# Performance work log

Hardware: AMD Instinct MI355X
Metric: run time of the kernel (lower is better)

## Reference

```python
import jax, jax.numpy as jnp
import numpy as np

B, N, K, H, D = 2, 8192, 16, 4, 32
C_IN, C_OUT = 64, 128
HD = H * D


def setup_inputs() -> dict:
    key = jax.random.key(0)
    ks = jax.random.split(key, 16)
    s = 0.02
    return {
        "xyzs": jax.random.normal(ks[0], (B, N, 3), jnp.float32),
        "features": jax.random.normal(ks[1], (B, N, C_IN), jnp.float32),
        "k_graph": jax.random.randint(ks[2], (B, N, K), 0, N),
        # projections (stored as [in, out]; torch Linear applies x @ W.T)
        "Wk": jax.random.normal(ks[3], (C_IN, HD), jnp.float32) * s,
        "Wv": jax.random.normal(ks[4], (C_IN, HD), jnp.float32) * s,
        "Wq": jax.random.normal(ks[5], (C_IN, HD), jnp.float32) * s,
        # aggregate MLP: Linear(HD,HD) -> ReLU -> Linear(HD,H)
        "A1": jax.random.normal(ks[6], (HD, HD), jnp.float32) * s,
        "b1": jnp.zeros((HD,), jnp.float32),
        "A2": jax.random.normal(ks[7], (HD, H), jnp.float32) * s,
        "b2": jnp.zeros((H,), jnp.float32),
        # position MLP: Linear(3,3) -> ReLU -> Linear(3,HD)
        "P1": jax.random.normal(ks[8], (3, 3), jnp.float32) * s,
        "bp1": jnp.zeros((3,), jnp.float32),
        "P2": jax.random.normal(ks[9], (3, HD), jnp.float32) * s,
        "bp2": jnp.zeros((HD,), jnp.float32),
        # output projection Linear(HD, C_OUT)
        "Wout": jax.random.normal(ks[10], (HD, C_OUT), jnp.float32) * s,
        "bout": jnp.zeros((C_OUT,), jnp.float32),
    }


def reference(xyzs, features, k_graph, Wk, Wv, Wq, A1, b1, A2, b2,
              P1, bp1, P2, bp2, Wout, bout):
    # KNN gather (irregular access): [B,N,K,*]
    nbr_feat = jax.vmap(lambda f, g: f[g])(features, k_graph)   # [B,N,K,C_IN]
    nbr_xyz = jax.vmap(lambda x, g: x[g])(xyzs, k_graph)        # [B,N,K,3]

    rel_pos = xyzs[:, :, None, :] - nbr_xyz                      # [B,N,K,3]
    pe = jax.nn.relu(rel_pos @ P1 + bp1) @ P2 + bp2              # [B,N,K,HD]

    keys = nbr_feat @ Wk                                         # [B,N,K,HD]
    values = nbr_feat @ Wv                                       # [B,N,K,HD]
    queries = features @ Wq                                      # [B,N,HD]

    # subtraction attention + aggregate MLP -> per-head logits
    attn = queries[:, :, None, :] - keys + pe                    # [B,N,K,HD]
    attn = jax.nn.relu(attn @ A1 + b1) @ A2 + b2                 # [B,N,K,H]
    attn = jax.nn.softmax(attn, axis=-2)                         # softmax over K

    # weighted reduce over neighbors
    fv = (values + pe).reshape(B, N, K, H, D)
    fused = jnp.sum(attn[..., None] * fv, axis=2)                # [B,N,H,D]
    fused = fused.reshape(B, N, HD)
    return fused @ Wout + bout                                   # [B,N,C_OUT]
```

## Files before the change

### kernel.cpp

```cpp
#include <hip/hip_runtime.h>
#include <hip/hip_bf16.h>

#define BATCH 2
#define NPTS  8192
#define BN    (BATCH * NPTS)
#define KNN   16
#define HEADS 4
#define HD    128
#define CIN   64
#define COUT  128
#define WCOLS 384

using short8  = __attribute__((ext_vector_type(8))) short;
using float4v = __attribute__((ext_vector_type(4))) float;
using float2v = __attribute__((ext_vector_type(2))) float;

static __device__ __forceinline__ unsigned short f2bf(float x) {
    unsigned u = __float_as_uint(x);
    u += 0x7fffu + ((u >> 16) & 1u);
    return (unsigned short)(u >> 16);
}
static __device__ __forceinline__ float bf_lo(unsigned u) { return __uint_as_float(u << 16); }
static __device__ __forceinline__ float bf_hi(unsigned u) { return __uint_as_float(u & 0xffff0000u); }
static __device__ __forceinline__ unsigned pack2(float a, float b) {
    return (unsigned)f2bf(a) | ((unsigned)f2bf(b) << 16);
}
static __device__ __forceinline__ float2v bf2pair(unsigned u) {
    float2v r;
    r.x = __uint_as_float(u << 16);
    r.y = __uint_as_float(u & 0xffff0000u);
    return r;
}

static __device__ __forceinline__ float2v pk_add(float2v a, float2v b) {
    float2v d;
    asm("v_pk_add_f32 %0, %1, %2" : "=v"(d) : "v"(a), "v"(b));
    return d;
}
static __device__ __forceinline__ float2v pk_sub(float2v a, float2v b) {
    float2v d;
    asm("v_pk_add_f32 %0, %1, %2 neg_lo:[0,1] neg_hi:[0,1]" : "=v"(d) : "v"(a), "v"(b));
    return d;
}
static __device__ __forceinline__ float2v pk_mul(float2v a, float2v b) {
    float2v d;
    asm("v_pk_mul_f32 %0, %1, %2" : "=v"(d) : "v"(a), "v"(b));
    return d;
}
static __device__ __forceinline__ float2v pk_fma(float2v a, float2v b, float2v c) {
    float2v d;
    asm("v_pk_fma_f32 %0, %1, %2, %3" : "=v"(d) : "v"(a), "v"(b), "v"(c));
    return d;
}
static __device__ __forceinline__ float2v sx2(float2v v, int mask) {
    float2v r;
    r.x = __shfl_xor(v.x, mask, 64);
    r.y = __shfl_xor(v.y, mask, 64);
    return r;
}

template <int CTRL>
static __device__ __forceinline__ float dpp_mov(float x) {
    return __int_as_float(
        __builtin_amdgcn_update_dpp(0, __float_as_int(x), CTRL, 0xf, 0xf, false));
}
static __device__ __forceinline__ float ror_sum16(float x) {
    x += dpp_mov<0x128>(x);
    x += dpp_mov<0x124>(x);
    x += dpp_mov<0x122>(x);
    x += dpp_mov<0x121>(x);
    return x;
}
static __device__ __forceinline__ float ror_max16(float x) {
    x = fmaxf(x, dpp_mov<0x128>(x));
    x = fmaxf(x, dpp_mov<0x124>(x));
    x = fmaxf(x, dpp_mov<0x122>(x));
    x = fmaxf(x, dpp_mov<0x121>(x));
    return x;
}

__global__ void prep_kernel(const float* __restrict__ Wk,
                            const float* __restrict__ Wv,
                            const float* __restrict__ Wq,
                            const float* __restrict__ A1,
                            const float* __restrict__ b1,
                            const float* __restrict__ P2,
                            const float* __restrict__ bp2,
                            const float* __restrict__ Wout,
                            unsigned short* __restrict__ WcatT,
                            unsigned short* __restrict__ WoutT,
                            float* __restrict__ P2A1,
                            float* __restrict__ cvec) {
    int t = blockIdx.x * blockDim.x + threadIdx.x;
    if (t < WCOLS * CIN) {
        int n = t >> 6, kk = t & 63;
        float val;
        if (n < 2 * HD) {
            const float* w = (n < HD ? Wq : Wk) + kk * HD;
            int jj = n & (HD - 1);
            float acc = 0.f;
            #pragma unroll 4
            for (int m = 0; m < HD; m += 4) {
                float4 wr = *(const float4*)(w + m);
                acc += wr.x * A1[(m+0)*HD + jj] + wr.y * A1[(m+1)*HD + jj]
                     + wr.z * A1[(m+2)*HD + jj] + wr.w * A1[(m+3)*HD + jj];
            }
            val = acc;
        } else {
            val = Wv[kk * HD + (n - 2 * HD)];
        }
        WcatT[t] = f2bf(val);
    } else if (t < WCOLS * CIN + COUT * HD) {
        int u = t - WCOLS * CIN;
        int n = u >> 7, kk = u & 127;
        WoutT[u] = f2bf(Wout[kk * COUT + n]);
    } else if (t < WCOLS * CIN + COUT * HD + 3 * HD) {
        int u = t - (WCOLS * CIN + COUT * HD);
        int r = u / HD, j = u % HD;
        const float* w = P2 + r * HD;
        float acc = 0.f;
        #pragma unroll 4
        for (int m = 0; m < HD; m += 4) {
            float4 wr = *(const float4*)(w + m);
            acc += wr.x * A1[(m+0)*HD + j] + wr.y * A1[(m+1)*HD + j]
                 + wr.z * A1[(m+2)*HD + j] + wr.w * A1[(m+3)*HD + j];
        }
        P2A1[u] = acc;
    } else if (t < WCOLS * CIN + COUT * HD + 3 * HD + HD) {
        int j = t - (WCOLS * CIN + COUT * HD + 3 * HD);
        float acc = b1[j];
        #pragma unroll 4
        for (int m = 0; m < HD; m += 4) {
            float4 wr = *(const float4*)(bp2 + m);
            acc += wr.x * A1[(m+0)*HD + j] + wr.y * A1[(m+1)*HD + j]
                 + wr.z * A1[(m+2)*HD + j] + wr.w * A1[(m+3)*HD + j];
        }
        cvec[j] = acc;
    }
}

#define AK 88
__global__ __launch_bounds__(256) void qkv_kernel(const float* __restrict__ F,
                                                  const unsigned short* __restrict__ WcatT,
                                                  const float* __restrict__ cvec,
                                                  unsigned short* __restrict__ QKVb) {
    __shared__ unsigned short Af[64 * AK];
    __shared__ unsigned short Bf[WCOLS * AK];
    int p0 = blockIdx.x * 64;
    int t = threadIdx.x;

    #pragma unroll
    for (int i = 0; i < 4; ++i) {
        int v = t + i * 256;
        int row = v >> 4, c4 = (v & 15) * 4;
        float4 fa = *(const float4*)(F + (p0 + row) * CIN + c4);
        uint2 u = make_uint2(pack2(fa.x, fa.y), pack2(fa.z, fa.w));
        *(uint2*)(&Af[row * AK + c4]) = u;
    }
    #pragma unroll
    for (int i = 0; i < 12; ++i) {
        int v = t + i * 256;
        int n = v >> 3, j16 = v & 7;
        *(uint4*)(&Bf[n * AK + j16 * 8]) = ((const uint4*)WcatT)[v];
    }
    __syncthreads();

    int w = t >> 6, l = t & 63;
    int ml = l & 15, quad = l >> 4;
    int m0 = w * 16;

    short8 a0 = *(const short8*)(&Af[(m0 + ml) * AK + quad * 8]);
    short8 a1 = *(const short8*)(&Af[(m0 + ml) * AK + 32 + quad * 8]);

    #pragma unroll
    for (int nt = 0; nt < 24; ++nt) {
        short8 b0 = *(const short8*)(&Bf[(nt * 16 + ml) * AK + quad * 8]);
        short8 b1 = *(const short8*)(&Bf[(nt * 16 + ml) * AK + 32 + quad * 8]);
        float4v acc = {0.f, 0.f, 0.f, 0.f};
        acc = __builtin_amdgcn_mfma_f32_16x16x32_bf16(a0, b0, acc, 0, 0, 0);
        acc = __builtin_amdgcn_mfma_f32_16x16x32_bf16(a1, b1, acc, 0, 0, 0);
        int n = nt * 16 + ml;
        float cadd = (n < HD) ? cvec[n] : 0.f;
        #pragma unroll
        for (int r = 0; r < 4; ++r) {
            int row = p0 + m0 + quad * 4 + r;
            QKVb[row * WCOLS + n] = f2bf(acc[r] + cadd);
        }
    }
}

__global__ __launch_bounds__(256) void attn_kernel(
        const float* __restrict__ xyzs, const int* __restrict__ kg,
        const unsigned short* __restrict__ QKVb,
        const float* __restrict__ P1, const float* __restrict__ bp1,
        const float* __restrict__ P2, const float* __restrict__ bp2,
        const float* __restrict__ P2A1,
        const float* __restrict__ A2, const float* __restrict__ b2,
        unsigned short* __restrict__ FUSEDb) {
    __shared__ float4 A2pA[64];
    __shared__ float4 A2pB[64];
    __shared__ float4 WApA[64];
    __shared__ float2 WApB[64];
    __shared__ float4 P2s[HD];
    int t = threadIdx.x;
    if (t < 64) {
        int c = t * 2;
        float4 a2l = *(const float4*)(A2 + c * 4);
        float4 a2h = *(const float4*)(A2 + (c + 1) * 4);
        A2pA[t] = make_float4(a2l.x, a2h.x, a2l.y, a2h.y);
        A2pB[t] = make_float4(a2l.z, a2h.z, a2l.w, a2h.w);
        WApA[t] = make_float4(P2A1[c], P2A1[c + 1], P2A1[HD + c], P2A1[HD + c + 1]);
        WApB[t] = make_float2(P2A1[2 * HD + c], P2A1[2 * HD + c + 1]);
    }
    if (t < HD) P2s[t] = make_float4(P2[t], P2[HD + t], P2[2 * HD + t], bp2[t]);
    __syncthreads();

    int lane = t & 63;
    int p = blockIdx.x * 4 + (t >> 6);
    int b = p >> 13;
    int k = lane & 15, cg = lane >> 4;
    int c0 = cg * 32;

    int idx = kg[p * KNN + k];
    int q = b * NPTS + idx;

    float r0 = xyzs[p * 3 + 0] - xyzs[q * 3 + 0];
    float r1 = xyzs[p * 3 + 1] - xyzs[q * 3 + 1];
    float r2 = xyzs[p * 3 + 2] - xyzs[q * 3 + 2];
    float h0 = fmaxf(r0 * P1[0] + r1 * P1[3] + r2 * P1[6] + bp1[0], 0.f);
    float h1 = fmaxf(r0 * P1[1] + r1 * P1[4] + r2 * P1[7] + bp1[1], 0.f);
    float h2 = fmaxf(r0 * P1[2] + r1 * P1[5] + r2 * P1[8] + bp1[2], 0.f);

    const uint4* qp = (const uint4*)(QKVb + (size_t)p * WCOLS + c0);
    const uint4* kp = (const uint4*)(QKVb + (size_t)q * WCOLS + HD + c0);
    const uint4* vp = (const uint4*)(QKVb + (size_t)q * WCOLS + 2 * HD + c0);
    uint4 quA[4] = {qp[0], qp[1], qp[2], qp[3]};
    uint4 kuA[4] = {kp[0], kp[1], kp[2], kp[3]};
    uint4 vuA[4] = {vp[0], vp[1], vp[2], vp[3]};

    float2v h0p = {h0, h0}, h1p = {h1, h1}, h2p = {h2, h2};
    float2v pl0 = {0.f, 0.f}, pl1 = {0.f, 0.f}, pl2 = {0.f, 0.f}, pl3 = {0.f, 0.f};
    int pbase = cg * 16;

    #pragma unroll
    for (int jc = 0; jc < 4; ++jc) {
        const unsigned* uq = (const unsigned*)&quA[jc];
        const unsigned* uk = (const unsigned*)&kuA[jc];
        #pragma unroll
        for (int jp = 0; jp < 4; ++jp) {
            float2v qp2 = bf2pair(uq[jp]);
            float2v kp2 = bf2pair(uk[jp]);
            int pi = pbase + jc * 4 + jp;
            float4 wa = WApA[pi];
            float2 wb = WApB[pi];
            float2v acc = pk_sub(qp2, kp2);
            acc = pk_fma(h0p, (float2v){wa.x, wa.y}, acc);
            acc = pk_fma(h1p, (float2v){wa.z, wa.w}, acc);
            acc = pk_fma(h2p, (float2v){wb.x, wb.y}, acc);
            float2v z2;
            z2.x = fmaxf(acc.x, 0.f);
            z2.y = fmaxf(acc.y, 0.f);
            float4 aA = A2pA[pi], aB = A2pB[pi];
            pl0 = pk_fma(z2, (float2v){aA.x, aA.y}, pl0);
            pl1 = pk_fma(z2, (float2v){aA.z, aA.w}, pl1);
            pl2 = pk_fma(z2, (float2v){aB.x, aB.y}, pl2);
            pl3 = pk_fma(z2, (float2v){aB.z, aB.w}, pl3);
        }
    }
    float l0 = pl0.x + pl0.y;
    float l1 = pl1.x + pl1.y;
    float l2 = pl2.x + pl2.y;
    float l3 = pl3.x + pl3.y;

    l0 += __shfl_xor(l0, 16, 64); l0 += __shfl_xor(l0, 32, 64);
    l1 += __shfl_xor(l1, 16, 64); l1 += __shfl_xor(l1, 32, 64);
    l2 += __shfl_xor(l2, 16, 64); l2 += __shfl_xor(l2, 32, 64);
    l3 += __shfl_xor(l3, 16, 64); l3 += __shfl_xor(l3, 32, 64);

    float lgt = l0;
    lgt = (cg == 1) ? l1 : lgt;
    lgt = (cg == 2) ? l2 : lgt;
    lgt = (cg == 3) ? l3 : lgt;

    float m16 = ror_max16(lgt);
    float e = __expf(lgt - m16);
    float s = ror_sum16(e);
    float a = e / s;

    float hb0 = ror_sum16(a * h0);
    float hb1 = ror_sum16(a * h1);
    float hb2 = ror_sum16(a * h2);

    float2v ap = {a, a};
    float2v y0[4], y1[4], y2[4], y3[4];
    {
        const unsigned* v0 = (const unsigned*)&vuA[0];
        const unsigned* v1 = (const unsigned*)&vuA[1];
        const unsigned* v2 = (const unsigned*)&vuA[2];
        const unsigned* v3 = (const unsigned*)&vuA[3];
        #pragma unroll
        for (int i = 0; i < 4; ++i) {
            y0[i] = pk_mul(ap, bf2pair(v0[i]));
            y1[i] = pk_mul(ap, bf2pair(v1[i]));
            y2[i] = pk_mul(ap, bf2pair(v2[i]));
            y3[i] = pk_mul(ap, bf2pair(v3[i]));
        }
    }
    bool hi3 = (k & 8) != 0;
    float2v k0[4], k1[4];
    #pragma unroll
    for (int i = 0; i < 4; ++i) {
        float2v s0 = hi3 ? y0[i] : y2[i];
        float2v s1 = hi3 ? y1[i] : y3[i];
        float2v r0v = sx2(s0, 8);
        float2v r1v = sx2(s1, 8);
        k0[i] = pk_add(hi3 ? y2[i] : y0[i], r0v);
        k1[i] = pk_add(hi3 ? y3[i] : y1[i], r1v);
    }
    bool hi2 = (k & 4) != 0;
    float2v m2[4];
    #pragma unroll
    for (int i = 0; i < 4; ++i) {
        float2v sv = hi2 ? k0[i] : k1[i];
        float2v rv = sx2(sv, 4);
        m2[i] = pk_add(hi2 ? k1[i] : k0[i], rv);
    }
    #pragma unroll
    for (int i = 0; i < 4; ++i) m2[i] = pk_add(m2[i], sx2(m2[i], 2));
    #pragma unroll
    for (int i = 0; i < 4; ++i) m2[i] = pk_add(m2[i], sx2(m2[i], 1));

    if ((k & 3) == 0) {
        int jc = k >> 2;
        float f[8];
        #pragma unroll
        for (int i = 0; i < 4; ++i) {
            float4 pp0 = P2s[c0 + jc * 8 + 2 * i];
            float4 pp1 = P2s[c0 + jc * 8 + 2 * i + 1];
            f[2 * i]     = m2[i].x + hb0 * pp0.x + hb1 * pp0.y + hb2 * pp0.z + pp0.w;
            f[2 * i + 1] = m2[i].y + hb0 * pp1.x + hb1 * pp1.y + hb2 * pp1.z + pp1.w;
        }
        uint4 fu;
        fu.x = pack2(f[0], f[1]); fu.y = pack2(f[2], f[3]);
        fu.z = pack2(f[4], f[5]); fu.w = pack2(f[6], f[7]);
        *(uint4*)(FUSEDb + (size_t)p * HD + c0 + jc * 8) = fu;
    }
}

#define OK2 144
__global__ __launch_bounds__(256) void out_kernel(const unsigned short* __restrict__ FUSEDb,
                                                  const unsigned short* __restrict__ WoutT,
                                                  const float* __restrict__ bout,
                                                  float* __restrict__ out) {
    __shared__ unsigned short Af[64 * OK2];
    __shared__ unsigned short Bf[HD * OK2];
    int p0 = blockIdx.x * 64;
    int t = threadIdx.x;

    #pragma unroll
    for (int i = 0; i < 4; ++i) {
        int v = t + i * 256;
        int row = v >> 4, j16 = v & 15;
        *(uint4*)(&Af[row * OK2 + j16 * 8]) = ((const uint4*)FUSEDb)[(p0 + row) * 16 + j16];
    }
    #pragma unroll
    for (int i = 0; i < 8; ++i) {
        int v = t + i * 256;
        int n = v >> 4, j16 = v & 15;
        *(uint4*)(&Bf[n * OK2 + j16 * 8]) = ((const uint4*)WoutT)[v];
    }
    __syncthreads();

    int w = t >> 6, l = t & 63;
    int ml = l & 15, quad = l >> 4;
    int m0 = w * 16;

    short8 af[4];
    #pragma unroll
    for (int ks = 0; ks < 4; ++ks)
        af[ks] = *(const short8*)(&Af[(m0 + ml) * OK2 + ks * 32 + quad * 8]);

    #pragma unroll
    for (int nt = 0; nt < 8; ++nt) {
        float4v acc = {0.f, 0.f, 0.f, 0.f};
        #pragma unroll
        for (int ks = 0; ks < 4; ++ks) {
            short8 bf = *(const short8*)(&Bf[(nt * 16 + ml) * OK2 + ks * 32 + quad * 8]);
            acc = __builtin_amdgcn_mfma_f32_16x16x32_bf16(af[ks], bf, acc, 0, 0, 0);
        }
        int n = nt * 16 + ml;
        float bo = bout[n];
        #pragma unroll
        for (int r = 0; r < 4; ++r) {
            int row = p0 + m0 + quad * 4 + r;
            out[row * COUT + n] = acc[r] + bo;
        }
    }
}

extern "C" void kernel_launch(void* const* d_in, const int* in_sizes, int n_in,
                              void* d_out, int out_size, void* d_ws, size_t ws_size,
                              hipStream_t stream) {
    const float* xyzs = (const float*)d_in[0];
    const float* feat = (const float*)d_in[1];
    const int*   kg   = (const int*)  d_in[2];
    const float* Wk   = (const float*)d_in[3];
    const float* Wv   = (const float*)d_in[4];
    const float* Wq   = (const float*)d_in[5];
    const float* A1   = (const float*)d_in[6];
    const float* b1   = (const float*)d_in[7];
    const float* A2   = (const float*)d_in[8];
    const float* b2   = (const float*)d_in[9];
    const float* P1   = (const float*)d_in[10];
    const float* bp1  = (const float*)d_in[11];
    const float* P2   = (const float*)d_in[12];
    const float* bp2  = (const float*)d_in[13];
    const float* Wout = (const float*)d_in[14];
    const float* bout = (const float*)d_in[15];
    float* out = (float*)d_out;

    float* ws = (float*)d_ws;
    float* cvec = ws;
    float* P2A1 = ws + 128;
    unsigned short* QKVb  = (unsigned short*)(ws + 512);
    unsigned short* FUSEDb = QKVb + (size_t)BN * WCOLS;
    unsigned short* WcatT = FUSEDb + (size_t)BN * HD;
    unsigned short* WoutT = WcatT + WCOLS * CIN;

    int prep_elems = WCOLS*CIN + COUT*HD + 3*HD + HD;
    prep_kernel<<<(prep_elems + 255) / 256, 256, 0, stream>>>(
        Wk, Wv, Wq, A1, b1, P2, bp2, Wout, WcatT, WoutT, P2A1, cvec);

    qkv_kernel<<<BN / 64, 256, 0, stream>>>(feat, WcatT, cvec, QKVb);

    attn_kernel<<<BN / 4, 256, 0, stream>>>(
        xyzs, kg, QKVb, P1, bp1, P2, bp2, P2A1, A2, b2, FUSEDb);

    out_kernel<<<BN / 64, 256, 0, stream>>>(FUSEDb, WoutT, bout, out);
}
```

Measured before the change: 133.9 us.

## Remap attn lanes to channel-slice by neighbor-group with padded xyz gather

Reorganizes the attention kernel so each lane owns an 8-channel slice across four neighbors instead of one neighbor across 32 channels. Key/value loads become one 16-byte load per neighbor per lane, logits are reduced with a butterfly transpose, and the V-weighted sum is done with in-lane FMAs plus two cross-group shuffles. xyz is repacked into float4 in the prep kernel so neighbor positions come from single vector loads, and the bf16 packing uses the hardware convert instruction. The goal is fewer shuffle reductions and more coalesced gathers. The cost is more shuffles in the softmax stage and higher register pressure.

```diff
diff --git a/kernel.cpp b/kernel.cpp
--- a/kernel.cpp
+++ b/kernel.cpp
@@ -58,25 +58,10 @@
     r.y = __shfl_xor(v.y, mask, 64);
     return r;
 }
-
-template <int CTRL>
-static __device__ __forceinline__ float dpp_mov(float x) {
-    return __int_as_float(
-        __builtin_amdgcn_update_dpp(0, __float_as_int(x), CTRL, 0xf, 0xf, false));
-}
-static __device__ __forceinline__ float ror_sum16(float x) {
-    x += dpp_mov<0x128>(x);
-    x += dpp_mov<0x124>(x);
-    x += dpp_mov<0x122>(x);
-    x += dpp_mov<0x121>(x);
-    return x;
-}
-static __device__ __forceinline__ float ror_max16(float x) {
-    x = fmaxf(x, dpp_mov<0x128>(x));
-    x = fmaxf(x, dpp_mov<0x124>(x));
-    x = fmaxf(x, dpp_mov<0x122>(x));
-    x = fmaxf(x, dpp_mov<0x121>(x));
-    return x;
+static __device__ __forceinline__ unsigned cvt_pk_bf16(float lo, float hi) {
+    unsigned r;
+    asm("v_cvt_pk_bf16_f32 %0, %1, %2" : "=v"(r) : "v"(lo), "v"(hi));
+    return r;
 }
 
 __global__ void prep_kernel(const float* __restrict__ Wk,
@@ -87,10 +72,12 @@
                             const float* __restrict__ P2,
                             const float* __restrict__ bp2,
                             const float* __restrict__ Wout,
+                            const float* __restrict__ xyzs,
                             unsigned short* __restrict__ WcatT,
                             unsigned short* __restrict__ WoutT,
                             float* __restrict__ P2A1,
-                            float* __restrict__ cvec) {
+                            float* __restrict__ cvec,
+                            float4* __restrict__ xyz4) {
     int t = blockIdx.x * blockDim.x + threadIdx.x;
     if (t < WCOLS * CIN) {
         int n = t >> 6, kk = t & 63;
@@ -136,6 +123,9 @@
                  + wr.z * A1[(m+2)*HD + j] + wr.w * A1[(m+3)*HD + j];
         }
         cvec[j] = acc;
+    } else if (t < WCOLS * CIN + COUT * HD + 3 * HD + HD + BN) {
+        int u = t - (WCOLS * CIN + COUT * HD + 3 * HD + HD);
+        xyz4[u] = make_float4(xyzs[u*3], xyzs[u*3+1], xyzs[u*3+2], 0.f);
     }
 }
 
@@ -190,7 +180,7 @@
 }
 
 __global__ __launch_bounds__(256) void attn_kernel(
-        const float* __restrict__ xyzs, const int* __restrict__ kg,
+        const float4* __restrict__ xyz4, const int* __restrict__ kg,
         const unsigned short* __restrict__ QKVb,
         const float* __restrict__ P1, const float* __restrict__ bp1,
         const float* __restrict__ P2, const float* __restrict__ bp2,
@@ -218,132 +208,164 @@
     int lane = t & 63;
     int p = blockIdx.x * 4 + (t >> 6);
     int b = p >> 13;
-    int k = lane & 15, cg = lane >> 4;
-    int c0 = cg * 32;
-
-    int idx = kg[p * KNN + k];
-    int q = b * NPTS + idx;
-
-    float r0 = xyzs[p * 3 + 0] - xyzs[q * 3 + 0];
-    float r1 = xyzs[p * 3 + 1] - xyzs[q * 3 + 1];
-    float r2 = xyzs[p * 3 + 2] - xyzs[q * 3 + 2];
-    float h0 = fmaxf(r0 * P1[0] + r1 * P1[3] + r2 * P1[6] + bp1[0], 0.f);
-    float h1 = fmaxf(r0 * P1[1] + r1 * P1[4] + r2 * P1[7] + bp1[1], 0.f);
-    float h2 = fmaxf(r0 * P1[2] + r1 * P1[5] + r2 * P1[8] + bp1[2], 0.f);
-
-    const uint4* qp = (const uint4*)(QKVb + (size_t)p * WCOLS + c0);
-    const uint4* kp = (const uint4*)(QKVb + (size_t)q * WCOLS + HD + c0);
-    const uint4* vp = (const uint4*)(QKVb + (size_t)q * WCOLS + 2 * HD + c0);
-    uint4 quA[4] = {qp[0], qp[1], qp[2], qp[3]};
-    uint4 kuA[4] = {kp[0], kp[1], kp[2], kp[3]};
-    uint4 vuA[4] = {vp[0], vp[1], vp[2], vp[3]};
-
-    float2v h0p = {h0, h0}, h1p = {h1, h1}, h2p = {h2, h2};
-    float2v pl0 = {0.f, 0.f}, pl1 = {0.f, 0.f}, pl2 = {0.f, 0.f}, pl3 = {0.f, 0.f};
-    int pbase = cg * 16;
-
-    #pragma unroll
-    for (int jc = 0; jc < 4; ++jc) {
-        const unsigned* uq = (const unsigned*)&quA[jc];
-        const unsigned* uk = (const unsigned*)&kuA[jc];
+    int cs = lane & 15, g = lane >> 4;
+
+    int qn[4];
+    #pragma unroll
+    for (int i = 0; i < 4; ++i) qn[i] = b * NPTS + kg[p * KNN + i * 4 + g];
+
+    float4 pw = xyz4[p];
+    float h0v[4], h1v[4], h2v[4];
+    #pragma unroll
+    for (int i = 0; i < 4; ++i) {
+        float4 qw = xyz4[qn[i]];
+        float r0 = pw.x - qw.x, r1 = pw.y - qw.y, r2 = pw.z - qw.z;
+        h0v[i] = fmaxf(r0*P1[0] + r1*P1[3] + r2*P1[6] + bp1[0], 0.f);
+        h1v[i] = fmaxf(r0*P1[1] + r1*P1[4] + r2*P1[7] + bp1[1], 0.f);
+        h2v[i] = fmaxf(r0*P1[2] + r1*P1[5] + r2*P1[8] + bp1[2], 0.f);
+    }
+
+    uint4 qu = *(const uint4*)(QKVb + (size_t)p * WCOLS + cs * 8);
+    uint4 ku[4];
+    #pragma unroll
+    for (int i = 0; i < 4; ++i)
+        ku[i] = *(const uint4*)(QKVb + (size_t)qn[i] * WCOLS + HD + cs * 8);
+
+    float2v hs0[4], hs1[4], hs2[4];
+    #pragma unroll
+    for (int i = 0; i < 4; ++i) {
+        hs0[i] = (float2v){h0v[i], h0v[i]};
+        hs1[i] = (float2v){h1v[i], h1v[i]};
+        hs2[i] = (float2v){h2v[i], h2v[i]};
+    }
+
+    float2v pl0[4], pl1[4], pl2[4], pl3[4];
+    #pragma unroll
+    for (int i = 0; i < 4; ++i) {
+        pl0[i] = (float2v){0.f, 0.f}; pl1[i] = (float2v){0.f, 0.f};
+        pl2[i] = (float2v){0.f, 0.f}; pl3[i] = (float2v){0.f, 0.f};
+    }
+    const unsigned* uq = (const unsigned*)&qu;
+    #pragma unroll
+    for (int jp = 0; jp < 4; ++jp) {
+        int pi = cs * 4 + jp;
+        float2v q2 = bf2pair(uq[jp]);
+        float4 wa = WApA[pi];
+        float2 wb = WApB[pi];
+        float4 aA = A2pA[pi], aB = A2pB[pi];
+        float2v wa01 = {wa.x, wa.y}, wa23 = {wa.z, wa.w}, wb01 = {wb.x, wb.y};
+        float2v aA01 = {aA.x, aA.y}, aA23 = {aA.z, aA.w};
+        float2v aB01 = {aB.x, aB.y}, aB23 = {aB.z, aB.w};
         #pragma unroll
-        for (int jp = 0; jp < 4; ++jp) {
-            float2v qp2 = bf2pair(uq[jp]);
-            float2v kp2 = bf2pair(uk[jp]);
-            int pi = pbase + jc * 4 + jp;
-            float4 wa = WApA[pi];
-            float2 wb = WApB[pi];
-            float2v acc = pk_sub(qp2, kp2);
-            acc = pk_fma(h0p, (float2v){wa.x, wa.y}, acc);
-            acc = pk_fma(h1p, (float2v){wa.z, wa.w}, acc);
-            acc = pk_fma(h2p, (float2v){wb.x, wb.y}, acc);
+        for (int i = 0; i < 4; ++i) {
+            float2v k2 = bf2pair(((const unsigned*)&ku[i])[jp]);
+            float2v acc = pk_sub(q2, k2);
+            acc = pk_fma(hs0[i], wa01, acc);
+            acc = pk_fma(hs1[i], wa23, acc);
+            acc = pk_fma(hs2[i], wb01, acc);
             float2v z2;
             z2.x = fmaxf(acc.x, 0.f);
             z2.y = fmaxf(acc.y, 0.f);
-            float4 aA = A2pA[pi], aB = A2pB[pi];
-            pl0 = pk_fma(z2, (float2v){aA.x, aA.y}, pl0);
-            pl1 = pk_fma(z2, (float2v){aA.z, aA.w}, pl1);
-            pl2 = pk_fma(z2, (float2v){aB.x, aB.y}, pl2);
-            pl3 = pk_fma(z2, (float2v){aB.z, aB.w}, pl3);
-        }
-    }
-    float l0 = pl0.x + pl0.y;
-    float l1 = pl1.x + pl1.y;
-    float l2 = pl2.x + pl2.y;
-    float l3 = pl3.x + pl3.y;
-
-    l0 += __shfl_xor(l0, 16, 64); l0 += __shfl_xor(l0, 32, 64);
-    l1 += __shfl_xor(l1, 16, 64); l1 += __shfl_xor(l1, 32, 64);
-    l2 += __shfl_xor(l2, 16, 64); l2 += __shfl_xor(l2, 32, 64);
-    l3 += __shfl_xor(l3, 16, 64); l3 += __shfl_xor(l3, 32, 64);
-
-    float lgt = l0;
-    lgt = (cg == 1) ? l1 : lgt;
-    lgt = (cg == 2) ? l2 : lgt;
-    lgt = (cg == 3) ? l3 : lgt;
-
-    float m16 = ror_max16(lgt);
-    float e = __expf(lgt - m16);
-    float s = ror_sum16(e);
-    float a = e / s;
-
-    float hb0 = ror_sum16(a * h0);
-    float hb1 = ror_sum16(a * h1);
-    float hb2 = ror_sum16(a * h2);
-
-    float2v ap = {a, a};
-    float2v y0[4], y1[4], y2[4], y3[4];
-    {
-        const unsigned* v0 = (const unsigned*)&vuA[0];
-        const unsigned* v1 = (const unsigned*)&vuA[1];
-        const unsigned* v2 = (const unsigned*)&vuA[2];
-        const unsigned* v3 = (const unsigned*)&vuA[3];
-        #pragma unroll
-        for (int i = 0; i < 4; ++i) {
-            y0[i] = pk_mul(ap, bf2pair(v0[i]));
-            y1[i] = pk_mul(ap, bf2pair(v1[i]));
-            y2[i] = pk_mul(ap, bf2pair(v2[i]));
-            y3[i] = pk_mul(ap, bf2pair(v3[i]));
-        }
-    }
-    bool hi3 = (k & 8) != 0;
-    float2v k0[4], k1[4];
-    #pragma unroll
-    for (int i = 0; i < 4; ++i) {
-        float2v s0 = hi3 ? y0[i] : y2[i];
-        float2v s1 = hi3 ? y1[i] : y3[i];
-        float2v r0v = sx2(s0, 8);
-        float2v r1v = sx2(s1, 8);
-        k0[i] = pk_add(hi3 ? y2[i] : y0[i], r0v);
-        k1[i] = pk_add(hi3 ? y3[i] : y1[i], r1v);
-    }
-    bool hi2 = (k & 4) != 0;
-    float2v m2[4];
-    #pragma unroll
-    for (int i = 0; i < 4; ++i) {
-        float2v sv = hi2 ? k0[i] : k1[i];
-        float2v rv = sx2(sv, 4);
-        m2[i] = pk_add(hi2 ? k1[i] : k0[i], rv);
-    }
-    #pragma unroll
-    for (int i = 0; i < 4; ++i) m2[i] = pk_add(m2[i], sx2(m2[i], 2));
-    #pragma unroll
-    for (int i = 0; i < 4; ++i) m2[i] = pk_add(m2[i], sx2(m2[i], 1));
-
-    if ((k & 3) == 0) {
-        int jc = k >> 2;
-        float f[8];
-        #pragma unroll
-        for (int i = 0; i < 4; ++i) {
-            float4 pp0 = P2s[c0 + jc * 8 + 2 * i];
-            float4 pp1 = P2s[c0 + jc * 8 + 2 * i + 1];
-            f[2 * i]     = m2[i].x + hb0 * pp0.x + hb1 * pp0.y + hb2 * pp0.z + pp0.w;
-            f[2 * i + 1] = m2[i].y + hb0 * pp1.x + hb1 * pp1.y + hb2 * pp1.z + pp1.w;
-        }
-        uint4 fu;
-        fu.x = pack2(f[0], f[1]); fu.y = pack2(f[2], f[3]);
-        fu.z = pack2(f[4], f[5]); fu.w = pack2(f[6], f[7]);
-        *(uint4*)(FUSEDb + (size_t)p * HD + c0 + jc * 8) = fu;
+            pl0[i] = pk_fma(z2, aA01, pl0[i]);
+            pl1[i] = pk_fma(z2, aA23, pl1[i]);
+            pl2[i] = pk_fma(z2, aB01, pl2[i]);
+            pl3[i] = pk_fma(z2, aB23, pl3[i]);
+        }
+    }
+
+    uint4 vu[4];
+    #pragma unroll
+    for (int i = 0; i < 4; ++i)
+        vu[i] = *(const uint4*)(QKVb + (size_t)qn[i] * WCOLS + 2 * HD + cs * 8);
+
+    float2v P[4], Qv[4];
+    #pragma unroll
+    for (int i = 0; i < 4; ++i) {
+        P[i]  = (float2v){pl0[i].x + pl0[i].y, pl1[i].x + pl1[i].y};
+        Qv[i] = (float2v){pl2[i].x + pl2[i].y, pl3[i].x + pl3[i].y};
+    }
+
+    bool hi8 = (cs & 8) != 0;
+    float2v kA = hi8 ? P[2]  : P[0],  sA = hi8 ? P[0]  : P[2];
+    float2v kB = hi8 ? Qv[2] : Qv[0], sB = hi8 ? Qv[0] : Qv[2];
+    float2v kC = hi8 ? P[3]  : P[1],  sC = hi8 ? P[1]  : P[3];
+    float2v kD = hi8 ? Qv[3] : Qv[1], sD = hi8 ? Qv[1] : Qv[3];
+    kA = pk_add(kA, sx2(sA, 8));
+    kB = pk_add(kB, sx2(sB, 8));
+    kC = pk_add(kC, sx2(sC, 8));
+    kD = pk_add(kD, sx2(sD, 8));
+    bool hi4 = (cs & 4) != 0;
+    float2v mP = hi4 ? kC : kA, sP = hi4 ? kA : kC;
+    float2v mQ = hi4 ? kD : kB, sQ = hi4 ? kB : kD;
+    mP = pk_add(mP, sx2(sP, 4));
+    mQ = pk_add(mQ, sx2(sQ, 4));
+    bool hi2 = (cs & 2) != 0;
+    float2v mT = hi2 ? mQ : mP, sT = hi2 ? mP : mQ;
+    mT = pk_add(mT, sx2(sT, 2));
+    bool hi1 = (cs & 1) != 0;
+    float Lm = hi1 ? mT.y : mT.x, Ls = hi1 ? mT.x : mT.y;
+    float L = Lm + __shfl_xor(Ls, 1, 64);
+
+    float mx = L;
+    mx = fmaxf(mx, __shfl_xor(mx, 4, 64));
+    mx = fmaxf(mx, __shfl_xor(mx, 8, 64));
+    mx = fmaxf(mx, __shfl_xor(mx, 16, 64));
+    mx = fmaxf(mx, __shfl_xor(mx, 32, 64));
+    float e = __expf(L - mx);
+    float ssum = e;
+    ssum += __shfl_xor(ssum, 4, 64);
+    ssum += __shfl_xor(ssum, 8, 64);
+    ssum += __shfl_xor(ssum, 16, 64);
+    ssum += __shfl_xor(ssum, 32, 64);
+    float a = e / ssum;
+
+    bool sb2 = (cs & 4) != 0, sb3 = (cs & 8) != 0;
+    float h0s = sb3 ? (sb2 ? h0v[3] : h0v[2]) : (sb2 ? h0v[1] : h0v[0]);
+    float h1s = sb3 ? (sb2 ? h1v[3] : h1v[2]) : (sb2 ? h1v[1] : h1v[0]);
+    float h2s = sb3 ? (sb2 ? h2v[3] : h2v[2]) : (sb2 ? h2v[1] : h2v[0]);
+    float ph0 = a * h0s, ph1 = a * h1s, ph2 = a * h2s;
+    ph0 += __shfl_xor(ph0, 4, 64);  ph1 += __shfl_xor(ph1, 4, 64);  ph2 += __shfl_xor(ph2, 4, 64);
+    ph0 += __shfl_xor(ph0, 8, 64);  ph1 += __shfl_xor(ph1, 8, 64);  ph2 += __shfl_xor(ph2, 8, 64);
+    ph0 += __shfl_xor(ph0, 16, 64); ph1 += __shfl_xor(ph1, 16, 64); ph2 += __shfl_xor(ph2, 16, 64);
+    ph0 += __shfl_xor(ph0, 32, 64); ph1 += __shfl_xor(ph1, 32, 64); ph2 += __shfl_xor(ph2, 32, 64);
+
+    float hq0 = __shfl(ph0, cs >> 2, 64);
+    float hq1 = __shfl(ph1, cs >> 2, 64);
+    float hq2 = __shfl(ph2, cs >> 2, 64);
+    int sbase = (lane & 48) | (cs >> 2);
+    float av0 = __shfl(a, sbase | (0 << 2), 64);
+    float av1 = __shfl(a, sbase | (1 << 2), 64);
+    float av2 = __shfl(a, sbase | (2 << 2), 64);
+    float av3 = __shfl(a, sbase | (3 << 2), 64);
+
+    float2v ap0 = {av0, av0}, ap1 = {av1, av1}, ap2 = {av2, av2}, ap3 = {av3, av3};
+    float2v wv[4];
+    #pragma unroll
+    for (int jp = 0; jp < 4; ++jp) {
+        float2v acc = pk_mul(ap0, bf2pair(((const unsigned*)&vu[0])[jp]));
+        acc = pk_fma(ap1, bf2pair(((const unsigned*)&vu[1])[jp]), acc);
+        acc = pk_fma(ap2, bf2pair(((const unsigned*)&vu[2])[jp]), acc);
+        acc = pk_fma(ap3, bf2pair(((const unsigned*)&vu[3])[jp]), acc);
+        wv[jp] = acc;
+    }
+    #pragma unroll
+    for (int jp = 0; jp < 4; ++jp) {
+        wv[jp] = pk_add(wv[jp], sx2(wv[jp], 16));
+        wv[jp] = pk_add(wv[jp], sx2(wv[jp], 32));
+    }
+
+    unsigned fw[4];
+    #pragma unroll
+    for (int jp = 0; jp < 4; ++jp) {
+        int ch0 = cs * 8 + 2 * jp;
+        float4 pA = P2s[ch0], pB = P2s[ch0 + 1];
+        float flo = wv[jp].x + hq0 * pA.x + hq1 * pA.y + hq2 * pA.z + pA.w;
+        float fhi = wv[jp].y + hq0 * pB.x + hq1 * pB.y + hq2 * pB.z + pB.w;
+        fw[jp] = cvt_pk_bf16(flo, fhi);
+    }
+    if (g == 0) {
+        uint4 fu = make_uint4(fw[0], fw[1], fw[2], fw[3]);
+        *(uint4*)(FUSEDb + (size_t)p * HD + cs * 8) = fu;
     }
 }
 
@@ -426,15 +448,16 @@
     unsigned short* FUSEDb = QKVb + (size_t)BN * WCOLS;
     unsigned short* WcatT = FUSEDb + (size_t)BN * HD;
     unsigned short* WoutT = WcatT + WCOLS * CIN;
-
-    int prep_elems = WCOLS*CIN + COUT*HD + 3*HD + HD;
+    float4* xyz4 = (float4*)(WoutT + COUT * HD);
+
+    int prep_elems = WCOLS*CIN + COUT*HD + 3*HD + HD + BN;
     prep_kernel<<<(prep_elems + 255) / 256, 256, 0, stream>>>(
-        Wk, Wv, Wq, A1, b1, P2, bp2, Wout, WcatT, WoutT, P2A1, cvec);
+        Wk, Wv, Wq, A1, b1, P2, bp2, Wout, xyzs, WcatT, WoutT, P2A1, cvec, xyz4);
 
     qkv_kernel<<<BN / 64, 256, 0, stream>>>(feat, WcatT, cvec, QKVb);
 
     attn_kernel<<<BN / 4, 256, 0, stream>>>(
-        xyzs, kg, QKVb, P1, bp1, P2, bp2, P2A1, A2, b2, FUSEDb);
+        xyz4, kg, QKVb, P1, bp1, P2, bp2, P2A1, A2, b2, FUSEDb);
 
     out_kernel<<<BN / 64, 256, 0, stream>>>(FUSEDb, WoutT, bout, out);
 }
```

After: 133.8 us. About the same (-0.1%).
